# Performance work log

Measured on AMD Instinct MI355X. Metric: run time of the kernel, lower is better.

Reference implementation:

```python
import jax, jax.numpy as jnp
import numpy as np

B = 512; S = 6; Q = 2            # meta-batch, n_way*k_shot, n_way*q_query
DIM = 64; IMG = 28; N_WAY = 2
HEADS = 4; HD = DIM // HEADS     # retrieval heads / head dim
EPS = 1e-5


def _pool_mat(inp, out):
    # exact torch AdaptiveAvgPool2d windowing as a matrix [out, inp]
    P = np.zeros((out, inp), np.float32)
    for i in range(out):
        s = (i * inp) // out
        e = -((-(i + 1) * inp) // out)
        P[i, s:e] = 1.0 / (e - s)
    return jnp.asarray(P)

P28 = _pool_mat(IMG, 8)  # 28 -> 8; subsequent 8 -> 8 pools are identity


def _gelu(x):
    return jax.nn.gelu(x, approximate=False)


def _conv(x, w, b):
    y = jax.lax.conv_general_dilated(x, w, (1, 1), ((1, 1), (1, 1)),
                                     dimension_numbers=('NCHW', 'OIHW', 'NCHW'))
    return y + b[None, :, None, None]


def _bn(x, p):
    # p rows: gamma, beta, running_mean, running_var (eval-mode BatchNorm2d)
    g, bt, m, v = p[0], p[1], p[2], p[3]
    sc = g / jnp.sqrt(v + EPS)
    return (x - m[None, :, None, None]) * sc[None, :, None, None] + bt[None, :, None, None]


def _img_in(x, c1w, c1b, bn1, c2w, c2b, bn2, c3w, c3b, bn3, c4w, c4b, bn4, lin_w):
    h = _bn(_conv(x, c1w, c1b), bn1)
    h = jnp.einsum('oi,ncij,pj->ncop', P28, h, P28)   # adaptive avg pool 28x28 -> 8x8
    h = _gelu(h)                                       # dropout is identity in eval
    h = _gelu(_bn(_conv(h, c2w, c2b), bn2))
    h = _gelu(_bn(_conv(h, c3w, c3b), bn3))
    h = _gelu(_bn(_conv(h, c4w, c4b), bn4))            # -> [N,1,8,8]
    h = h.reshape(h.shape[0], -1)                      # [N,64]
    return h @ lin_w.T                                 # Linear(64 -> DIM, no bias)


def _net(x, w1, w2):
    # x: [B,K,D]; w1,w2: [B,D,D] batched fast weights
    h = jnp.einsum('bed,bkd->bke', w1, x)
    ah = _gelu(h)
    y = jnp.einsum('bed,bkd->bke', w2, ah)
    return y, h


def _get_lor(x, w1, w2, r_q, r_k, r_v, r_o, ln_w, ln_b):
    b, k, _ = x.shape
    q, _ = _net(x, w1, w2)
    qh = jnp.einsum('nhd,bkd->bknh', r_q, q)
    sc = jnp.einsum('bknh,rnh->bknr', qh, r_k) / (HD ** 0.5)
    p = jax.nn.softmax(sc, axis=-1)
    lor = jnp.einsum('bknr,rnh->bknh', p, r_v).reshape(b, k, DIM)
    lor = jnp.einsum('de,bkd->bke', r_o, lor)
    z = lor + x
    mu = z.mean(-1, keepdims=True)
    var = ((z - mu) ** 2).mean(-1, keepdims=True)
    return (z - mu) / jnp.sqrt(var + EPS) * ln_w + ln_b


def _forward(query_w, sxs, qxs, inner_lr, c1w, c1b, bn1, c2w, c2b, bn2, c3w, c3b, bn3,
             c4w, c4b, bn4, lin_w, emb, w1, w2, tags, r_q, r_k, r_v, r_o, ln_w, ln_b,
             sys, qys):
    b = query_w.shape[0]
    s = sxs.shape[1]
    q = qxs.shape[1]
    feats = lambda im: _img_in(im.reshape(-1, 1, IMG, IMG), c1w, c1b, bn1, c2w, c2b,
                               bn2, c3w, c3b, bn3, c4w, c4b, bn4, lin_w)
    sx = feats(sxs).reshape(b, s, DIM)
    qx = feats(qxs).reshape(b, q, DIM)
    qe = tags[4]
    w1b = jnp.broadcast_to(w1, (b, DIM, DIM))
    w2b = jnp.broadcast_to(w2, (b, DIM, DIM))
    bound = sx + emb[sys]                                          # [B,S,D]
    # all 4 tag variants for all S shots in one vectorized get_lor call
    inp = (bound[:, :, None, :] + tags[:4][None, None]).reshape(b, s * 4, DIM)
    lors = _get_lor(inp, w1b, w2b, r_q, r_k, r_v, r_o, ln_w, ln_b).reshape(b, s, 4, DIM)
    l1s, r1s, l2s, r2s = lors[:, :, 0], lors[:, :, 1], lors[:, :, 2], lors[:, :, 3]
    qw1 = w1[None] + jnp.einsum('bsl,bsr->blr', l1s, r1s)
    qw2 = w2[None] + jnp.einsum('bsl,bsr->blr', l2s, r2s)
    preds, _ = _net(qx + qe, qw1, qw2)                             # [B,Q,D]
    logits = jnp.einsum('ld,bqd->bql', emb, preds).reshape(-1, N_WAY)
    labels = qys.reshape(-1)
    ls = jax.nn.log_softmax(logits)
    task_loss = -jnp.take_along_axis(ls, labels[:, None], axis=1).mean()
    n_correct = (jnp.argmax(logits, axis=1) == labels).sum()
    return task_loss, n_correct, b * q


def setup_inputs() -> dict:
    key = jax.random.key(0)
    ks = jax.random.split(key, 24)
    rn = lambda i, sh, sc=1.0: sc * jax.random.normal(ks[i], sh, jnp.float32)
    def bnp(i, c):
        k0, k1, k2 = jax.random.split(ks[i], 3)
        return jnp.stack([1.0 + 0.1 * jax.random.normal(k0, (c,)),
                          0.1 * jax.random.normal(k1, (c,)),
                          0.1 * jax.random.normal(k2, (c,)),
                          0.5 + jax.random.uniform(jax.random.fold_in(ks[i], 3), (c,))])
    return {
        'query_w': rn(0, (B, DIM)),
        'sxs': rn(1, (B, S, IMG * IMG)),
        'qxs': rn(2, (B, Q, IMG * IMG)),
        'inner_lr': jnp.float32(0.1),
        'c1w': rn(3, (32, 1, 3, 3), 0.3), 'c1b': rn(4, (32,), 0.1), 'bn1': bnp(5, 32),
        'c2w': rn(6, (32, 32, 3, 3), 0.06), 'c2b': rn(7, (32,), 0.1), 'bn2': bnp(8, 32),
        'c3w': rn(9, (32, 32, 3, 3), 0.06), 'c3b': rn(10, (32,), 0.1), 'bn3': bnp(11, 32),
        'c4w': rn(12, (1, 32, 3, 3), 0.06), 'c4b': rn(13, (1,), 0.1), 'bn4': bnp(14, 1),
        'lin_w': rn(15, (DIM, 64), 0.125),
        'emb': rn(16, (N_WAY, DIM), 0.125),
        'w1': rn(17, (DIM, DIM), 0.125),
        'w2': rn(18, (DIM, DIM), 0.125),
        'tags': rn(19, (8, DIM), 0.125),
        'r_q': rn(20, (HEADS, HD, DIM), 0.125),
        'r_k': rn(21, (16, HEADS, HD), 0.25),
        'r_v': rn(22, (16, HEADS, HD), 0.25),
        'r_o': rn(23, (DIM, DIM), 0.125),
        'ln_w': 0.001 * jnp.ones((DIM,), jnp.float32),
        'ln_b': jnp.zeros((DIM,), jnp.float32),
        'sys': jax.random.randint(jax.random.fold_in(key, 100), (B, S), 0, N_WAY),
        'qys': jax.random.randint(jax.random.fold_in(key, 101), (B, Q), 0, N_WAY),
    }


def reference(query_w, sxs, qxs, inner_lr, c1w, c1b, bn1, c2w, c2b, bn2, c3w, c3b, bn3,
              c4w, c4b, bn4, lin_w, emb, w1, w2, tags, r_q, r_k, r_v, r_o, ln_w, ln_b,
              sys, qys):
    task_loss, n_correct, n_q = _forward(query_w, sxs, qxs, inner_lr, c1w, c1b, bn1,
                                         c2w, c2b, bn2, c3w, c3b, bn3, c4w, c4b, bn4,
                                         lin_w, emb, w1, w2, tags, r_q, r_k, r_v, r_o,
                                         ln_w, ln_b, sys, qys)
    return (task_loss, task_loss, jnp.float32(0.0), n_correct, n_q)
```

## Files before the change

kernel.cpp:

```cpp
#include <hip/hip_runtime.h>
#include <math.h>

constexpr int NSUP = 3072;
constexpr float EPSF = 1e-5f;

constexpr int WS_W1B  = 0;
constexpr int WS_B1   = 1024;
constexpr int WS_W2B  = 1056;
constexpr int WS_W3B  = 5664;
constexpr int WS_W4B  = 10272;
constexpr int WS_B4   = 10416;
constexpr int WS_B2   = 10420;
constexpr int WS_B3   = 10452;
constexpr int WS_HW1  = 10484;
constexpr int WS_HW2  = 12788;
constexpr int WS_HRQ  = 15092;
constexpr int WS_HROT = 17396;
constexpr int WS_RKB  = 19700;
constexpr int WS_RVT  = 20212;
constexpr int WS_PART = 20724;
constexpr int WS_FEATS= 21748;

using short8 = __attribute__((ext_vector_type(8))) short;
using f32x4  = __attribute__((ext_vector_type(4))) float;

__device__ __forceinline__ float gelu_f(float x) {
    float z  = fabsf(x) * 0.70710678118654752440f;
    float t  = __builtin_amdgcn_rcpf(__builtin_fmaf(0.3275911f, z, 1.0f));
    float p  = t * __builtin_fmaf(t,
                 __builtin_fmaf(t,
                   __builtin_fmaf(t,
                     __builtin_fmaf(t, 1.061405429f, -1.453152027f),
                     1.421413741f),
                   -0.284496736f),
                 0.254829592f);
    float e  = __expf(-z * z);
// ... 8 lines not shown
__device__ __forceinline__ float bflo(unsigned u) { return __uint_as_float(u << 16); }
__device__ __forceinline__ float bfhi(unsigned u) { return __uint_as_float(u & 0xffff0000u); }

__global__ void __launch_bounds__(256) precompute_kernel(
    const float* __restrict__ c1w, const float* __restrict__ c1b, const float* __restrict__ bn1,
    const float* __restrict__ c2w, const float* __restrict__ c2b, const float* __restrict__ bn2,
    const float* __restrict__ c3w, const float* __restrict__ c3b, const float* __restrict__ bn3,
    const float* __restrict__ c4w, const float* __restrict__ c4b, const float* __restrict__ bn4,
    const float* __restrict__ w1, const float* __restrict__ w2,
    const float* __restrict__ rq, const float* __restrict__ ro,
    const float* __restrict__ rk, const float* __restrict__ rv,
    float* __restrict__ ws)
{
    const int gid = blockIdx.x * 256 + threadIdx.x;
    const int gsz = gridDim.x * 256;

    unsigned short* w1b = (unsigned short*)(ws + WS_W1B);
    for (int v = gid; v < 2048; v += gsz) {
        int c8 = v & 7, colx = (v >> 3) & 15, qd = (v >> 7) & 3, hh = (v >> 9) & 1, kt = v >> 10;
        int tap = kt * 32 + qd * 8 + c8;
        int oc = hh * 16 + colx;
        unsigned short o = 0;
        if (tap < 36) {
            int tt = tap / 6, s = tap - tt * 6;
            float sum = 0.f;
            for (int di = 0; di < 3; ++di) {
                int a = tt - di; if (a < 0 || a > 3) continue;
                for (int dj = 0; dj < 3; ++dj) {
                    int bb = s - dj; if (bb < 0 || bb > 3) continue;
                    sum += c1w[oc * 9 + di * 3 + dj];
// ... 21 lines not shown
        float sc2 = bn2[oc] * rsqrtf(bn2[96 + oc] + EPSF);
        float sc3 = bn3[oc] * rsqrtf(bn3[96 + oc] + EPSF);
        w2b[v] = f2bf(c2w[oc * 288 + ic * 9 + tap] * sc2);
        w3b[v] = f2bf(c3w[oc * 288 + ic * 9 + tap] * sc3);
    }
    {
        unsigned short* w4b = (unsigned short*)(ws + WS_W4B);
        float sc4 = bn4[0] * rsqrtf(bn4[3] + EPSF);
        for (int v = gid; v < 288; v += gsz) {
            int tap = v >> 5, ic = v & 31;
            w4b[v] = f2bf(c4w[ic * 9 + tap] * sc4);
        }
        if (gid == 0) ws[WS_B4] = (c4b[0] - bn4[2]) * sc4 + bn4[1];
    }
    unsigned short* hw1 = (unsigned short*)(ws + WS_HW1);
    unsigned short* hw2 = (unsigned short*)(ws + WS_HW2);
    unsigned short* hrq = (unsigned short*)(ws + WS_HRQ);
    unsigned short* hro = (unsigned short*)(ws + WS_HROT);
    for (int v = gid; v < 4608; v += gsz) {
        int e = v / 72, d = v - e * 72;
        unsigned short a = 0, b = 0, c = 0, r = 0;
        if (d < 64) {
            a = f2bf(w1[e * 64 + d]);
            b = f2bf(w2[e * 64 + d]);
            c = f2bf(rq[e * 64 + d]);
            r = f2bf(ro[d * 64 + e]);
        }
        hw1[v] = a; hw2[v] = b; hrq[v] = c; hro[v] = r;
    }
    unsigned short* rkb = (unsigned short*)(ws + WS_RKB);
    unsigned short* rvt = (unsigned short*)(ws + WS_RVT);
    for (int v = gid; v < 1024; v += gsz) {
        int nn = v >> 8, x = (v >> 4) & 15, y = v & 15;
        rkb[v] = f2bf(rk[x * 64 + nn * 16 + y] * 0.25f);
        rvt[v] = f2bf(rv[y * 64 + nn * 16 + x]);
    }
}

__device__ __forceinline__ void conv32g(const unsigned short* __restrict__ A,
                                        const unsigned short* __restrict__ Wg,
                                        int col, int quad, f32x4 (&acc)[4][2])
{
    int ab[4];
    #pragma unroll
    for (int mt = 0; mt < 4; ++mt) {
        int px = mt * 16 + col;
        ab[mt] = quad * 800 + ((px >> 3) * 10 + (px & 7)) * 8;
        acc[mt][0] = (f32x4){0,0,0,0};
        acc[mt][1] = (f32x4){0,0,0,0};
    }
    #pragma unroll
    for (int dr = 0; dr < 3; ++dr)
// ... 14 lines not shown
__device__ __forceinline__ void conv_store4(unsigned short* __restrict__ A,
                                            const f32x4 (&acc)[4][2],
                                            float bi0, float bi1, int col, int quad)
{
    #pragma unroll
    for (int mt = 0; mt < 4; ++mt)
        #pragma unroll
        for (int reg = 0; reg < 4; ++reg) {
            int px = mt * 16 + quad * 4 + reg;
            int P = ((px >> 3) + 1) * 10 + (px & 7) + 1;
            A[(col >> 3) * 800 + P * 8 + (col & 7)]       = f2bf(gelu_f(acc[mt][0][reg] + bi0));
            A[(2 + (col >> 3)) * 800 + P * 8 + (col & 7)] = f2bf(gelu_f(acc[mt][1][reg] + bi1));
        }
}

__global__ void __launch_bounds__(256, 4) feats_kernel(
    const float* __restrict__ sxs, const float* __restrict__ qxs,
    const float* __restrict__ lin_w, const float* __restrict__ ws,
    float* __restrict__ feats)
{
    __shared__ __align__(16) unsigned short sAct[4][3200];
    __shared__ __align__(16) float sh4[4][64];

    const int t    = threadIdx.x;
    const int wv   = t >> 6;
    const int lane = t & 63;
    const int col  = lane & 15;
    const int quad = lane >> 4;
    const int n    = blockIdx.x * 4 + wv;

    unsigned short* A = sAct[wv];

    float bi1a = ws[WS_B1 + col], bi1b = ws[WS_B1 + 16 + col];
    float bi2a = ws[WS_B2 + col], bi2b = ws[WS_B2 + 16 + col];
    float bi3a = ws[WS_B3 + col], bi3b = ws[WS_B3 + 16 + col];
    float b4   = ws[WS_B4];

    {
        const float* img = (n < NSUP) ? (sxs + (size_t)n * 784) : (qxs + (size_t)(n - NSUP) * 784);
        const float4* sv = (const float4*)img;
        #pragma unroll
        for (int j = 0; j < 4; ++j) {
            int idx = j * 64 + lane;
            if (idx < 196) {
                float4 v = sv[idx];
                ushort4 o = { f2bf(v.x), f2bf(v.y), f2bf(v.z), f2bf(v.w) };
                *(ushort4*)(A + idx * 4) = o;
            }
        }
    }

    f32x4 acc[4][2];
    {
        const unsigned short* w1g = (const unsigned short*)(ws + WS_W1B);
        short8 b00 = *(const short8*)(w1g + ((0 * 4 + quad) * 16 + col) * 8);
        short8 b01 = *(const short8*)(w1g + ((1 * 4 + quad) * 16 + col) * 8);
        short8 b10 = *(const short8*)(w1g + ((2 * 4 + quad) * 16 + col) * 8);
        short8 b11 = *(const short8*)(w1g + ((3 * 4 + quad) * 16 + col) * 8);
        int ttj[8], ssj[8];
        #pragma unroll
        for (int j = 0; j < 8; ++j) {
            int k = quad * 8 + j;
            ttj[j] = k / 6; ssj[j] = k - ttj[j] * 6;
        }
        #pragma unroll
        for (int mt = 0; mt < 4; ++mt) {
            acc[mt][0] = (f32x4){0,0,0,0};
            acc[mt][1] = (f32x4){0,0,0,0};
            int px = mt * 16 + col;
            int sr = (((px >> 3) * 7) >> 1) - 1;
            int sc = (((px & 7) * 7) >> 1) - 1;
            short8 a0;
            #pragma unroll
            for (int j = 0; j < 8; ++j) {
                int rr = sr + ttj[j], cc = sc + ssj[j];
                bool ok = ((unsigned)rr < 28u) && ((unsigned)cc < 28u);
                int off = ok ? (rr * 28 + cc) : 0;
                unsigned short hv = A[off];
                a0[j] = ok ? (short)hv : (short)0;
            }
            acc[mt][0] = __builtin_amdgcn_mfma_f32_16x16x32_bf16(a0, b00, acc[mt][0], 0, 0, 0);
            acc[mt][1] = __builtin_amdgcn_mfma_f32_16x16x32_bf16(a0, b01, acc[mt][1], 0, 0, 0);
            short8 a1 = {0,0,0,0,0,0,0,0};
            if (quad == 0) {
                #pragma unroll
                for (int j = 0; j < 4; ++j) {
                    int rr = sr + 5, cc = sc + 2 + j;
                    bool ok = ((unsigned)rr < 28u) && ((unsigned)cc < 28u);
                    int off = ok ? (rr * 28 + cc) : 0;
                    unsigned short hv = A[off];
                    a1[j] = ok ? (short)hv : (short)0;
                }
            }
            acc[mt][0] = __builtin_amdgcn_mfma_f32_16x16x32_bf16(a1, b10, acc[mt][0], 0, 0, 0);
            acc[mt][1] = __builtin_amdgcn_mfma_f32_16x16x32_bf16(a1, b11, acc[mt][1], 0, 0, 0);
        }
    }
    {
        uint4 z4 = {0, 0, 0, 0};
        #pragma unroll
        for (int it = 0; it < 3; ++it) {
            int h = lane + it * 64;
            if (h < 144) {
                int pi = h >> 2, ch = h & 3;
                int P;
                if (pi < 10)      P = pi;
                else if (pi < 20) P = 90 + (pi - 10);
                else { int k = pi - 20; int r = 1 + (k >> 1); P = r * 10 + (k & 1) * 9; }
                ((uint4*)A)[ch * 100 + P] = z4;
            }
        }
    }
    conv_store4(A, acc, bi1a, bi1b, col, quad);

    conv32g(A, (const unsigned short*)(ws + WS_W2B), col, quad, acc);
    conv_store4(A, acc, bi2a, bi2b, col, quad);
    conv32g(A, (const unsigned short*)(ws + WS_W3B), col, quad, acc);
    conv_store4(A, acc, bi3a, bi3b, col, quad);

    {
        f32x4 acc4[4];
        int ab[4];
        #pragma unroll
        for (int mt = 0; mt < 4; ++mt) {
            int px = mt * 16 + col;
            ab[mt] = quad * 800 + ((px >> 3) * 10 + (px & 7)) * 8;
            acc4[mt] = (f32x4){0,0,0,0};
        }
        const unsigned short* w4g = (const unsigned short*)(ws + WS_W4B);
        #pragma unroll
        for (int dr = 0; dr < 3; ++dr)
            #pragma unroll
            for (int dc = 0; dc < 3; ++dc) {
                int tap = dr * 3 + dc;
                short8 b = *(const short8*)(w4g + tap * 32 + quad * 8);
                #pragma unroll
                for (int mt = 0; mt < 4; ++mt) {
                    short8 a = *(const short8*)(A + ab[mt] + (dr * 10 + dc) * 8);
                    acc4[mt] = __builtin_amdgcn_mfma_f32_16x16x32_bf16(a, b, acc4[mt], 0, 0, 0);
                }
            }
        if (col < 4) {
            f32x4 v = acc4[0];
            if (col == 1) v = acc4[1];
            else if (col == 2) v = acc4[2];
            else if (col == 3) v = acc4[3];
            #pragma unroll
            for (int reg = 0; reg < 4; ++reg)
                sh4[wv][col * 16 + quad * 4 + reg] = gelu_f(v[reg] + b4);
        }
    }

    {
        const float4* lw = (const float4*)(lin_w + (size_t)lane * 64);
        const float4* hp = (const float4*)sh4[wv];
        float acc2 = 0.f;
        #pragma unroll
        for (int j = 0; j < 16; ++j) {
            float4 w = lw[j], h = hp[j];
            acc2 += w.x * h.x + w.y * h.y + w.z * h.z + w.w * h.w;
        }
        feats[n * 64 + lane] = acc2;
    }
}

__device__ __forceinline__ void head_gemm(const unsigned short* __restrict__ Ab,
                                          const unsigned short* __restrict__ Bw,
                                          int col, int quad, int wvid, f32x4 res[2])
{
    #pragma unroll
    for (int u = 0; u < 2; ++u) {
        int tau = wvid + u * 4;
        int mt = tau & 1, nt = tau >> 1;
        f32x4 acc = {0, 0, 0, 0};
        #pragma unroll
        for (int kt = 0; kt < 2; ++kt) {
            short8 a = *(const short8*)(Ab + (mt * 16 + col) * 72 + kt * 32 + quad * 8);
            short8 b = *(const short8*)(Bw + (nt * 16 + col) * 72 + kt * 32 + quad * 8);
            acc = __builtin_amdgcn_mfma_f32_16x16x32_bf16(a, b, acc, 0, 0, 0);
        }
        res[u] = acc;
    }
}

__global__ void __launch_bounds__(256, 2) head_kernel(
    const float* __restrict__ emb, const float* __restrict__ tags,
    const float* __restrict__ lnw, const float* __restrict__ lnb,
    const int* __restrict__ sys, const int* __restrict__ qys,
    const float* __restrict__ ws, const float* __restrict__ feats,
    float* __restrict__ part)
{
    __shared__ __align__(16) unsigned short sW1B[4608], sW2B[4608], sRQB[4608], sROT[4608];
    __shared__ __align__(16) unsigned short bufA[2304], bufB[2304];
    __shared__ __align__(16) unsigned short sP[2048];
    __shared__ __align__(16) float sXf[1536];
    __shared__ __align__(16) float s_xq[128], s_ah[128], s_yp[128];
    __shared__ float s_t1[12], s_t2[12], s_mu[24], s_rs[24], s_lg[4];

    const int t    = threadIdx.x;
    const int b    = blockIdx.x;
    const int wvid = t >> 6;
    const int col  = t & 15;
    const int quad = (t >> 4) & 3;

    for (int i = t; i < 576; i += 256) {
        ((uint4*)sW1B)[i] = ((const uint4*)(ws + WS_HW1))[i];
        ((uint4*)sW2B)[i] = ((const uint4*)(ws + WS_HW2))[i];
        ((uint4*)sRQB)[i] = ((const uint4*)(ws + WS_HRQ))[i];
        ((uint4*)sROT)[i] = ((const uint4*)(ws + WS_HROT))[i];
    }
    {
        uint4 z = {0, 0, 0, 0};
        if (t < 72) {
            ((uint4*)(bufA + 1728))[t] = z;
            ((uint4*)(bufB + 1728))[t] = z;
        }
        if (t < 64)
            ((uint4*)(sP + 1536))[t] = z;
    }
    for (int idx = t; idx < 1536; idx += 256) {
        int k = idx >> 6, e = idx & 63;
        int s = k >> 2, tg = k & 3;
        int cls = sys[b * 6 + s];
        float v = feats[(b * 6 + s) * 64 + e] + emb[cls * 64 + e] + tags[tg * 64 + e];
        sXf[idx] = v;
        bufA[k * 72 + e] = f2bf(v);
    }
    __syncthreads();

    f32x4 r[2];
    head_gemm(bufA, sW1B, col, quad, wvid, r);
    #pragma unroll
    for (int u = 0; u < 2; ++u) {
        int tau = wvid + u * 4, mt = tau & 1, nt = tau >> 1;
        #pragma unroll
        for (int reg = 0; reg < 4; ++reg) {
            int row = mt * 16 + quad * 4 + reg;
            if (row < 24) bufB[row * 72 + nt * 16 + col] = f2bf(gelu_f(r[u][reg]));
        }
    }
    __syncthreads();
    head_gemm(bufB, sW2B, col, quad, wvid, r);
    #pragma unroll
    for (int u = 0; u < 2; ++u) {
        int tau = wvid + u * 4, mt = tau & 1, nt = tau >> 1;
        #pragma unroll
        for (int reg = 0; reg < 4; ++reg) {
            int row = mt * 16 + quad * 4 + reg;
            if (row < 24) bufA[row * 72 + nt * 16 + col] = f2bf(r[u][reg]);
        }
    }
    __syncthreads();
    head_gemm(bufA, sRQB, col, quad, wvid, r);
    #pragma unroll
    for (int u = 0; u < 2; ++u) {
        int tau = wvid + u * 4, mt = tau & 1, nt = tau >> 1;
        #pragma unroll
        for (int reg = 0; reg < 4; ++reg) {
            int row = mt * 16 + quad * 4 + reg;
            if (row < 24) bufB[row * 72 + nt * 16 + col] = f2bf(r[u][reg]);
        }
    }
    __syncthreads();

    {
        const int nh = wvid;
        const unsigned short* rkB = (const unsigned short*)(ws + WS_RKB) + nh * 256;
        const unsigned short* rvT = (const unsigned short*)(ws + WS_RVT) + nh * 256;
        const short8 zz = {0,0,0,0,0,0,0,0};
        const bool lo = (quad < 2);
        short8 bK = lo ? *(const short8*)(rkB + col * 16 + quad * 8) : zz;
        short8 a0 = lo ? *(const short8*)(bufB + col * 72 + nh * 16 + quad * 8) : zz;
        short8 a1 = lo ? *(const short8*)(bufB + (16 + col) * 72 + nh * 16 + quad * 8) : zz;
        f32x4 s0 = __builtin_amdgcn_mfma_f32_16x16x32_bf16(a0, bK, (f32x4){0,0,0,0}, 0, 0, 0);
        f32x4 s1 = __builtin_amdgcn_mfma_f32_16x16x32_bf16(a1, bK, (f32x4){0,0,0,0}, 0, 0, 0);
        #pragma unroll
        for (int reg = 0; reg < 4; ++reg) {
            float v = s0[reg];
            float m = v;
            m = fmaxf(m, __shfl_xor(m, 1)); m = fmaxf(m, __shfl_xor(m, 2));
            m = fmaxf(m, __shfl_xor(m, 4)); m = fmaxf(m, __shfl_xor(m, 8));
            float p = __expf(v - m);
            float su = p;
            su += __shfl_xor(su, 1); su += __shfl_xor(su, 2);
            su += __shfl_xor(su, 4); su += __shfl_xor(su, 8);
            sP[(quad * 4 + reg) * 64 + nh * 16 + col] = f2bf(p / su);
            v = s1[reg];
            m = v;
// ... 7 lines not shown
        }
        short8 bV  = lo ? *(const short8*)(rvT + col * 16 + quad * 8) : zz;
        short8 pa0 = lo ? *(const short8*)(sP + col * 64 + nh * 16 + quad * 8) : zz;
        short8 pa1 = lo ? *(const short8*)(sP + (16 + col) * 64 + nh * 16 + quad * 8) : zz;
        f32x4 o0 = __builtin_amdgcn_mfma_f32_16x16x32_bf16(pa0, bV, (f32x4){0,0,0,0}, 0, 0, 0);
        f32x4 o1 = __builtin_amdgcn_mfma_f32_16x16x32_bf16(pa1, bV, (f32x4){0,0,0,0}, 0, 0, 0);
        #pragma unroll
        for (int reg = 0; reg < 4; ++reg) {
            bufA[(quad * 4 + reg) * 72 + nh * 16 + col] = f2bf(o0[reg]);
            int tok = 16 + quad * 4 + reg;
            if (tok < 24) bufA[tok * 72 + nh * 16 + col] = f2bf(o1[reg]);
        }
    }
    __syncthreads();

    head_gemm(bufA, sROT, col, quad, wvid, r);
    #pragma unroll
    for (int u = 0; u < 2; ++u) {
        int tau = wvid + u * 4, mt = tau & 1, nt = tau >> 1;
        #pragma unroll
        for (int reg = 0; reg < 4; ++reg) {
            int row = mt * 16 + quad * 4 + reg;
            if (row < 24) {
                int idx = row * 64 + nt * 16 + col;
                sXf[idx] = sXf[idx] + r[u][reg];
            }
        }
    }
    __syncthreads();

    if (t < 192) {
        int k = t >> 3, j = t & 7;
        const float4* zp = (const float4*)(sXf + k * 64 + j * 8);
        float4 v0 = zp[0], v1 = zp[1];
        float sx_ = v0.x + v0.y + v0.z + v0.w + v1.x + v1.y + v1.z + v1.w;
        sx_ += __shfl_xor(sx_, 1); sx_ += __shfl_xor(sx_, 2); sx_ += __shfl_xor(sx_, 4);
        float mu = sx_ * (1.0f / 64.0f);
        float d0 = v0.x - mu, d1 = v0.y - mu, d2 = v0.z - mu, d3 = v0.w - mu;
        float d4 = v1.x - mu, d5 = v1.y - mu, d6 = v1.z - mu, d7 = v1.w - mu;
        float vv = d0*d0 + d1*d1 + d2*d2 + d3*d3 + d4*d4 + d5*d5 + d6*d6 + d7*d7;
        vv += __shfl_xor(vv, 1); vv += __shfl_xor(vv, 2); vv += __shfl_xor(vv, 4);
        if (j == 0) {
            s_mu[k] = mu;
            s_rs[k] = 1.0f / sqrtf(vv * (1.0f / 64.0f) + EPSF);
        }
    }
    __syncthreads();
    for (int idx = t; idx < 1536; idx += 256) {
        int k = idx >> 6, e = idx & 63;
        float v = (sXf[idx] - s_mu[k]) * s_rs[k] * lnw[e] + lnb[e];
        bufB[k * 72 + e] = f2bf(v);
    }
    if (t < 128) {
        int q = t >> 6, e = t & 63;
        s_xq[t] = feats[(NSUP + b * 2 + q) * 64 + e] + tags[256 + e];
    }
    __syncthreads();

    if (t < 96) {
        int idx = t >> 3, j = t & 7;
        int q = idx / 6, s = idx - q * 6;
        uint4 u = ((const uint4*)(bufB + (s * 4 + 1) * 72))[j];
        const float* x = s_xq + q * 64 + j * 8;
        float d = bflo(u.x)*x[0] + bfhi(u.x)*x[1] + bflo(u.y)*x[2] + bfhi(u.y)*x[3]
                + bflo(u.z)*x[4] + bfhi(u.z)*x[5] + bflo(u.w)*x[6] + bfhi(u.w)*x[7];
        d += __shfl_xor(d, 1); d += __shfl_xor(d, 2); d += __shfl_xor(d, 4);
        if (j == 0) s_t1[idx] = d;
    }
    __syncthreads();
    if (t < 128) {
        int q = t >> 6, e = t & 63;
        const uint4* wp = (const uint4*)(sW1B + e * 72);
        const float* xp = s_xq + q * 64;
        float acc = 0.f;
        #pragma unroll
        for (int j = 0; j < 8; ++j) {
            uint4 u = wp[j];
            const float* x = xp + j * 8;
            acc += bflo(u.x)*x[0] + bfhi(u.x)*x[1] + bflo(u.y)*x[2] + bfhi(u.y)*x[3]
                 + bflo(u.z)*x[4] + bfhi(u.z)*x[5] + bflo(u.w)*x[6] + bfhi(u.w)*x[7];
        }
        #pragma unroll
        for (int s = 0; s < 6; ++s)
            acc += bflo((unsigned)bufB[(s * 4 + 0) * 72 + e]) * s_t1[q * 6 + s];
        s_ah[t] = gelu_f(acc);
    }
    __syncthreads();
    if (t < 96) {
        int idx = t >> 3, j = t & 7;
        int q = idx / 6, s = idx - q * 6;
        uint4 u = ((const uint4*)(bufB + (s * 4 + 3) * 72))[j];
        const float* x = s_ah + q * 64 + j * 8;
        float d = bflo(u.x)*x[0] + bfhi(u.x)*x[1] + bflo(u.y)*x[2] + bfhi(u.y)*x[3]
                + bflo(u.z)*x[4] + bfhi(u.z)*x[5] + bflo(u.w)*x[6] + bfhi(u.w)*x[7];
        d += __shfl_xor(d, 1); d += __shfl_xor(d, 2); d += __shfl_xor(d, 4);
        if (j == 0) s_t2[idx] = d;
    }
    __syncthreads();
    if (t < 128) {
        int q = t >> 6, e = t & 63;
        const uint4* wp = (const uint4*)(sW2B + e * 72);
        const float* xp = s_ah + q * 64;
        float acc = 0.f;
        #pragma unroll
        for (int j = 0; j < 8; ++j) {
            uint4 u = wp[j];
            const float* x = xp + j * 8;
            acc += bflo(u.x)*x[0] + bfhi(u.x)*x[1] + bflo(u.y)*x[2] + bfhi(u.y)*x[3]
                 + bflo(u.z)*x[4] + bfhi(u.z)*x[5] + bflo(u.w)*x[6] + bfhi(u.w)*x[7];
        }
        #pragma unroll
        for (int s = 0; s < 6; ++s)
            acc += bflo((unsigned)bufB[(s * 4 + 2) * 72 + e]) * s_t2[q * 6 + s];
        s_yp[t] = acc;
    }
    __syncthreads();
    if (t < 32) {
        int q = t >> 4, ll = (t >> 3) & 1, j = t & 7;
        const float* ep = emb + ll * 64 + j * 8;
        const float* yp = s_yp + q * 64 + j * 8;
        float d = ep[0]*yp[0] + ep[1]*yp[1] + ep[2]*yp[2] + ep[3]*yp[3]
                + ep[4]*yp[4] + ep[5]*yp[5] + ep[6]*yp[6] + ep[7]*yp[7];
        d += __shfl_xor(d, 1); d += __shfl_xor(d, 2); d += __shfl_xor(d, 4);
        if (j == 0) s_lg[q * 2 + ll] = d;
    }
    __syncthreads();
    if (t == 0) {
        float lsum = 0.f, corr = 0.f;
        #pragma unroll
        for (int q = 0; q < 2; ++q) {
            float l0 = s_lg[q * 2], l1 = s_lg[q * 2 + 1];
            int lab = qys[b * 2 + q];
            float m = fmaxf(l0, l1);
            float lse = m + logf(expf(l0 - m) + expf(l1 - m));
            lsum += -((lab ? l1 : l0) - lse);
            int pred = (l1 > l0) ? 1 : 0;
            corr += (pred == lab) ? 1.0f : 0.0f;
        }
        part[b] = lsum;
        part[512 + b] = corr;
    }
}

__global__ void __launch_bounds__(256) finalize_kernel(const float* __restrict__ part,
                                                       float* __restrict__ out)
{
    __shared__ float sl[256], sc[256];
    const int t = threadIdx.x;
    sl[t] = part[t] + part[t + 256];
    sc[t] = part[512 + t] + part[768 + t];
    __syncthreads();
    for (int s = 128; s > 0; s >>= 1) {
        if (t < s) { sl[t] += sl[t + s]; sc[t] += sc[t + s]; }
        __syncthreads();
    }
    if (t == 0) {
        float loss = sl[0] * (1.0f / 1024.0f);
        out[0] = loss;
        out[1] = loss;
        out[2] = 0.0f;
        out[3] = sc[0];
        out[4] = 1024.0f;
    }
}

extern "C" void kernel_launch(void* const* d_in, const int* in_sizes, int n_in,
                              void* d_out, int out_size, void* d_ws, size_t ws_size,
                              hipStream_t stream)
{
    (void)in_sizes; (void)n_in; (void)out_size; (void)ws_size;
    const float* sxs  = (const float*)d_in[1];
    const float* qxs  = (const float*)d_in[2];
    const float* c1w  = (const float*)d_in[4];
    const float* c1b  = (const float*)d_in[5];
    const float* bn1  = (const float*)d_in[6];
    const float* c2w  = (const float*)d_in[7];
    const float* c2b  = (const float*)d_in[8];
// ... 12 lines not shown
    const float* rq   = (const float*)d_in[21];
    const float* rk   = (const float*)d_in[22];
    const float* rv   = (const float*)d_in[23];
    const float* ro   = (const float*)d_in[24];
    const float* lnw  = (const float*)d_in[25];
    const float* lnb  = (const float*)d_in[26];
    const int*   sys  = (const int*)d_in[27];
    const int*   qys  = (const int*)d_in[28];

    float* ws  = (float*)d_ws;
    float* out = (float*)d_out;

    precompute_kernel<<<64, 256, 0, stream>>>(c1w, c1b, bn1, c2w, c2b, bn2,
                                              c3w, c3b, bn3, c4w, c4b, bn4,
                                              w1, w2, rq, ro, rk, rv, ws);
    feats_kernel<<<1024, 256, 0, stream>>>(sxs, qxs, lin_w, ws, ws + WS_FEATS);
    head_kernel<<<512, 256, 0, stream>>>(emb, tags, lnw, lnb, sys, qys,
                                         ws, ws + WS_FEATS, ws + WS_PART);
    finalize_kernel<<<1, 256, 0, stream>>>(ws + WS_PART, out);
}
```

Before: 167.8 us.

## Fuse feature extraction, head, and finalize into one per-task kernel

Merges the conv feature kernel, the per-task head kernel and the final reduction into a single 512-thread kernel per meta-batch task. Each of the eight waves extracts one image's features straight into shared memory, so the global feats round trip and two launches go away. The last block, found through an atomic counter, does the final reduction. The rq·w2 product is also folded into a precomputed matrix, which removes one head GEMM stage. In exchange, shared memory per block grows via a union, and the finalize step now relies on threadfence and atomic ordering.

```diff
diff --git a/kernel.cpp b/kernel.cpp
--- a/kernel.cpp
+++ b/kernel.cpp
@@ -1,7 +1,6 @@
 #include <hip/hip_runtime.h>
 #include <math.h>
 
-constexpr int NSUP = 3072;
 constexpr float EPSF = 1e-5f;
 
 constexpr int WS_W1B  = 0;
@@ -13,13 +12,13 @@
 constexpr int WS_B2   = 10420;
 constexpr int WS_B3   = 10452;
 constexpr int WS_HW1  = 10484;
-constexpr int WS_HW2  = 12788;
-constexpr int WS_HRQ  = 15092;
+constexpr int WS_HM   = 12788;
+constexpr int WS_HW2  = 15092;
 constexpr int WS_HROT = 17396;
 constexpr int WS_RKB  = 19700;
 constexpr int WS_RVT  = 20212;
 constexpr int WS_PART = 20724;
-constexpr int WS_FEATS= 21748;
+constexpr int WS_CNT  = 21748;
 
 using short8 = __attribute__((ext_vector_type(8))) short;
 using f32x4  = __attribute__((ext_vector_type(4))) float;
@@ -58,6 +57,8 @@
 {
     const int gid = blockIdx.x * 256 + threadIdx.x;
     const int gsz = gridDim.x * 256;
+
+    if (gid == 0) *((unsigned*)(ws + WS_CNT)) = 0u;
 
     unsigned short* w1b = (unsigned short*)(ws + WS_W1B);
     for (int v = gid; v < 2048; v += gsz) {
@@ -109,8 +110,8 @@
         if (gid == 0) ws[WS_B4] = (c4b[0] - bn4[2]) * sc4 + bn4[1];
     }
     unsigned short* hw1 = (unsigned short*)(ws + WS_HW1);
+    unsigned short* hm  = (unsigned short*)(ws + WS_HM);
     unsigned short* hw2 = (unsigned short*)(ws + WS_HW2);
-    unsigned short* hrq = (unsigned short*)(ws + WS_HRQ);
     unsigned short* hro = (unsigned short*)(ws + WS_HROT);
     for (int v = gid; v < 4608; v += gsz) {
         int e = v / 72, d = v - e * 72;
@@ -118,10 +119,12 @@
         if (d < 64) {
             a = f2bf(w1[e * 64 + d]);
             b = f2bf(w2[e * 64 + d]);
-            c = f2bf(rq[e * 64 + d]);
+            float m = 0.f;
+            for (int q = 0; q < 64; ++q) m += rq[e * 64 + q] * w2[q * 64 + d];
+            c = f2bf(m);
             r = f2bf(ro[d * 64 + e]);
         }
-        hw1[v] = a; hw2[v] = b; hrq[v] = c; hro[v] = r;
+        hw1[v] = a; hw2[v] = b; hm[v] = c; hro[v] = r;
     }
     unsigned short* rkb = (unsigned short*)(ws + WS_RKB);
     unsigned short* rvt = (unsigned short*)(ws + WS_RVT);
@@ -131,6 +134,24 @@
         rvt[v] = f2bf(rv[y * 64 + nn * 16 + x]);
     }
 }
+
+struct FeatsSmem {
+    unsigned short sAct[8][3200];
+    float          sh4[8][64];
+};
+struct HeadSmem {
+    unsigned short sW1B[4608];
+    unsigned short sM[4608];
+    unsigned short sW2B[4608];
+    unsigned short sROT[4608];
+    unsigned short bufA[2304];
+    unsigned short bufB[2304];
+    unsigned short sP[2048];
+};
+union FusedSmem {
+    FeatsSmem f;
+    HeadSmem  h;
+};
 
 __device__ __forceinline__ void conv32g(const unsigned short* __restrict__ A,
                                         const unsigned short* __restrict__ Wg,
@@ -175,264 +196,240 @@
         }
 }
 
-__global__ void __launch_bounds__(256, 4) feats_kernel(
+__device__ __forceinline__ f32x4 head_gemm8(const unsigned short* __restrict__ Ab,
+                                            const unsigned short* __restrict__ Bw,
+                                            int col, int quad, int wvid)
+{
+    int mt = wvid & 1, nt = wvid >> 1;
+    f32x4 acc = {0, 0, 0, 0};
+    #pragma unroll
+    for (int kt = 0; kt < 2; ++kt) {
+        short8 a = *(const short8*)(Ab + (mt * 16 + col) * 72 + kt * 32 + quad * 8);
+        short8 b = *(const short8*)(Bw + (nt * 16 + col) * 72 + kt * 32 + quad * 8);
+        acc = __builtin_amdgcn_mfma_f32_16x16x32_bf16(a, b, acc, 0, 0, 0);
+    }
+    return acc;
+}
+
+__global__ void __launch_bounds__(512, 4) fused_kernel(
     const float* __restrict__ sxs, const float* __restrict__ qxs,
-    const float* __restrict__ lin_w, const float* __restrict__ ws,
-    float* __restrict__ feats)
+    const float* __restrict__ lin_w,
+    const float* __restrict__ emb, const float* __restrict__ tags,
+    const float* __restrict__ lnw, const float* __restrict__ lnb,
+    const int* __restrict__ sys, const int* __restrict__ qys,
+    float* __restrict__ ws, float* __restrict__ out)
 {
-    __shared__ __align__(16) unsigned short sAct[4][3200];
-    __shared__ __align__(16) float sh4[4][64];
+    __shared__ __align__(16) FusedSmem sm;
+    __shared__ __align__(16) float sFeat[8][64];
+    __shared__ __align__(16) float sXf[1536];
+    __shared__ __align__(16) float s_xq[128], s_ah[128], s_yp[128];
+    __shared__ float s_t1[12], s_t2[12], s_mu[24], s_rs[24], s_lg[4], s_red[16];
+    __shared__ int s_last;
 
     const int t    = threadIdx.x;
+    const int b    = blockIdx.x;
     const int wv   = t >> 6;
     const int lane = t & 63;
     const int col  = lane & 15;
     const int quad = lane >> 4;
-    const int n    = blockIdx.x * 4 + wv;
-
-    unsigned short* A = sAct[wv];
-
-    float bi1a = ws[WS_B1 + col], bi1b = ws[WS_B1 + 16 + col];
-    float bi2a = ws[WS_B2 + col], bi2b = ws[WS_B2 + 16 + col];
-    float bi3a = ws[WS_B3 + col], bi3b = ws[WS_B3 + 16 + col];
-    float b4   = ws[WS_B4];
 
     {
-        const float* img = (n < NSUP) ? (sxs + (size_t)n * 784) : (qxs + (size_t)(n - NSUP) * 784);
-        const float4* sv = (const float4*)img;
-        #pragma unroll
-        for (int j = 0; j < 4; ++j) {
-            int idx = j * 64 + lane;
-            if (idx < 196) {
-                float4 v = sv[idx];
-                ushort4 o = { f2bf(v.x), f2bf(v.y), f2bf(v.z), f2bf(v.w) };
-                *(ushort4*)(A + idx * 4) = o;
-            }
-        }
-    }
-
-    f32x4 acc[4][2];
-    {
-        const unsigned short* w1g = (const unsigned short*)(ws + WS_W1B);
-        short8 b00 = *(const short8*)(w1g + ((0 * 4 + quad) * 16 + col) * 8);
-        short8 b01 = *(const short8*)(w1g + ((1 * 4 + quad) * 16 + col) * 8);
-        short8 b10 = *(const short8*)(w1g + ((2 * 4 + quad) * 16 + col) * 8);
-        short8 b11 = *(const short8*)(w1g + ((3 * 4 + quad) * 16 + col) * 8);
-        int ttj[8], ssj[8];
-        #pragma unroll
-        for (int j = 0; j < 8; ++j) {
-            int k = quad * 8 + j;
-            ttj[j] = k / 6; ssj[j] = k - ttj[j] * 6;
-        }
-        #pragma unroll
-        for (int mt = 0; mt < 4; ++mt) {
-            acc[mt][0] = (f32x4){0,0,0,0};
-            acc[mt][1] = (f32x4){0,0,0,0};
-            int px = mt * 16 + col;
-            int sr = (((px >> 3) * 7) >> 1) - 1;
-            int sc = (((px & 7) * 7) >> 1) - 1;
-            short8 a0;
+        unsigned short* A = sm.f.sAct[wv];
+        float bi1a = ws[WS_B1 + col], bi1b = ws[WS_B1 + 16 + col];
+        float bi2a = ws[WS_B2 + col], bi2b = ws[WS_B2 + 16 + col];
+        float bi3a = ws[WS_B3 + col], bi3b = ws[WS_B3 + 16 + col];
+        float b4   = ws[WS_B4];
+
+        {
+            const float* img = (wv < 6) ? (sxs + ((size_t)b * 6 + wv) * 784)
+                                        : (qxs + ((size_t)b * 2 + (wv - 6)) * 784);
+            const float4* sv = (const float4*)img;
+            #pragma unroll
+            for (int j = 0; j < 4; ++j) {
+                int idx = j * 64 + lane;
+                if (idx < 196) {
+                    float4 v = sv[idx];
+                    ushort4 o = { f2bf(v.x), f2bf(v.y), f2bf(v.z), f2bf(v.w) };
+                    *(ushort4*)(A + idx * 4) = o;
+                }
+            }
+        }
+
+        f32x4 acc[4][2];
+        {
+            const unsigned short* w1g = (const unsigned short*)(ws + WS_W1B);
+            short8 b00 = *(const short8*)(w1g + ((0 * 4 + quad) * 16 + col) * 8);
+            short8 b01 = *(const short8*)(w1g + ((1 * 4 + quad) * 16 + col) * 8);
+            short8 b10 = *(const short8*)(w1g + ((2 * 4 + quad) * 16 + col) * 8);
+            short8 b11 = *(const short8*)(w1g + ((3 * 4 + quad) * 16 + col) * 8);
+            int ttj[8], ssj[8];
             #pragma unroll
             for (int j = 0; j < 8; ++j) {
-                int rr = sr + ttj[j], cc = sc + ssj[j];
-                bool ok = ((unsigned)rr < 28u) && ((unsigned)cc < 28u);
-                int off = ok ? (rr * 28 + cc) : 0;
-                unsigned short hv = A[off];
-                a0[j] = ok ? (short)hv : (short)0;
-            }
-            acc[mt][0] = __builtin_amdgcn_mfma_f32_16x16x32_bf16(a0, b00, acc[mt][0], 0, 0, 0);
-            acc[mt][1] = __builtin_amdgcn_mfma_f32_16x16x32_bf16(a0, b01, acc[mt][1], 0, 0, 0);
-            short8 a1 = {0,0,0,0,0,0,0,0};
-            if (quad == 0) {
+                int k = quad * 8 + j;
+                ttj[j] = k / 6; ssj[j] = k - ttj[j] * 6;
+            }
+            #pragma unroll
+            for (int mt = 0; mt < 4; ++mt) {
+                acc[mt][0] = (f32x4){0,0,0,0};
+                acc[mt][1] = (f32x4){0,0,0,0};
+                int px = mt * 16 + col;
+                int sr = (((px >> 3) * 7) >> 1) - 1;
+                int sc = (((px & 7) * 7) >> 1) - 1;
+                short8 a0;
                 #pragma unroll
-                for (int j = 0; j < 4; ++j) {
-                    int rr = sr + 5, cc = sc + 2 + j;
+                for (int j = 0; j < 8; ++j) {
+                    int rr = sr + ttj[j], cc = sc + ssj[j];
                     bool ok = ((unsigned)rr < 28u) && ((unsigned)cc < 28u);
                     int off = ok ? (rr * 28 + cc) : 0;
                     unsigned short hv = A[off];
-                    a1[j] = ok ? (short)hv : (short)0;
+                    a0[j] = ok ? (short)hv : (short)0;
                 }
-            }
-            acc[mt][0] = __builtin_amdgcn_mfma_f32_16x16x32_bf16(a1, b10, acc[mt][0], 0, 0, 0);
-            acc[mt][1] = __builtin_amdgcn_mfma_f32_16x16x32_bf16(a1, b11, acc[mt][1], 0, 0, 0);
-        }
-    }
-    {
-        uint4 z4 = {0, 0, 0, 0};
-        #pragma unroll
-        for (int it = 0; it < 3; ++it) {
-            int h = lane + it * 64;
-            if (h < 144) {
-                int pi = h >> 2, ch = h & 3;
-                int P;
-                if (pi < 10)      P = pi;
-                else if (pi < 20) P = 90 + (pi - 10);
-                else { int k = pi - 20; int r = 1 + (k >> 1); P = r * 10 + (k & 1) * 9; }
-                ((uint4*)A)[ch * 100 + P] = z4;
-            }
-        }
-    }
-    conv_store4(A, acc, bi1a, bi1b, col, quad);
-
-    conv32g(A, (const unsigned short*)(ws + WS_W2B), col, quad, acc);
-    conv_store4(A, acc, bi2a, bi2b, col, quad);
-    conv32g(A, (const unsigned short*)(ws + WS_W3B), col, quad, acc);
-    conv_store4(A, acc, bi3a, bi3b, col, quad);
-
-    {
-        f32x4 acc4[4];
-        int ab[4];
-        #pragma unroll
-        for (int mt = 0; mt < 4; ++mt) {
-            int px = mt * 16 + col;
-            ab[mt] = quad * 800 + ((px >> 3) * 10 + (px & 7)) * 8;
-            acc4[mt] = (f32x4){0,0,0,0};
-        }
-        const unsigned short* w4g = (const unsigned short*)(ws + WS_W4B);
-        #pragma unroll
-        for (int dr = 0; dr < 3; ++dr)
-            #pragma unroll
-            for (int dc = 0; dc < 3; ++dc) {
-                int tap = dr * 3 + dc;
-                short8 b = *(const short8*)(w4g + tap * 32 + quad * 8);
+                acc[mt][0] = __builtin_amdgcn_mfma_f32_16x16x32_bf16(a0, b00, acc[mt][0], 0, 0, 0);
+                acc[mt][1] = __builtin_amdgcn_mfma_f32_16x16x32_bf16(a0, b01, acc[mt][1], 0, 0, 0);
+                short8 a1 = {0,0,0,0,0,0,0,0};
+                if (quad == 0) {
+                    #pragma unroll
+                    for (int j = 0; j < 4; ++j) {
+                        int rr = sr + 5, cc = sc + 2 + j;
+                        bool ok = ((unsigned)rr < 28u) && ((unsigned)cc < 28u);
+                        int off = ok ? (rr * 28 + cc) : 0;
+                        unsigned short hv = A[off];
+                        a1[j] = ok ? (short)hv : (short)0;
+                    }
+                }
+                acc[mt][0] = __builtin_amdgcn_mfma_f32_16x16x32_bf16(a1, b10, acc[mt][0], 0, 0, 0);
+                acc[mt][1] = __builtin_amdgcn_mfma_f32_16x16x32_bf16(a1, b11, acc[mt][1], 0, 0, 0);
+            }
+        }
+        {
+            uint4 z4 = {0, 0, 0, 0};
+            #pragma unroll
+            for (int it = 0; it < 3; ++it) {
+                int h = lane + it * 64;
+                if (h < 144) {
+                    int pi = h >> 2, ch = h & 3;
+                    int P;
+                    if (pi < 10)      P = pi;
+                    else if (pi < 20) P = 90 + (pi - 10);
+                    else { int k = pi - 20; int r = 1 + (k >> 1); P = r * 10 + (k & 1) * 9; }
+                    ((uint4*)A)[ch * 100 + P] = z4;
+                }
+            }
+        }
+        conv_store4(A, acc, bi1a, bi1b, col, quad);
+
+        conv32g(A, (const unsigned short*)(ws + WS_W2B), col, quad, acc);
+        conv_store4(A, acc, bi2a, bi2b, col, quad);
+        conv32g(A, (const unsigned short*)(ws + WS_W3B), col, quad, acc);
+        conv_store4(A, acc, bi3a, bi3b, col, quad);
+
+        {
+            f32x4 acc4[4];
+            int ab[4];
+            #pragma unroll
+            for (int mt = 0; mt < 4; ++mt) {
+                int px = mt * 16 + col;
+                ab[mt] = quad * 800 + ((px >> 3) * 10 + (px & 7)) * 8;
+                acc4[mt] = (f32x4){0,0,0,0};
+            }
+            const unsigned short* w4g = (const unsigned short*)(ws + WS_W4B);
+            #pragma unroll
+            for (int dr = 0; dr < 3; ++dr)
                 #pragma unroll
-                for (int mt = 0; mt < 4; ++mt) {
-                    short8 a = *(const short8*)(A + ab[mt] + (dr * 10 + dc) * 8);
-                    acc4[mt] = __builtin_amdgcn_mfma_f32_16x16x32_bf16(a, b, acc4[mt], 0, 0, 0);
+                for (int dc = 0; dc < 3; ++dc) {
+                    int tap = dr * 3 + dc;
+                    short8 bb = *(const short8*)(w4g + tap * 32 + quad * 8);
+                    #pragma unroll
+                    for (int mt = 0; mt < 4; ++mt) {
+                        short8 a = *(const short8*)(A + ab[mt] + (dr * 10 + dc) * 8);
+                        acc4[mt] = __builtin_amdgcn_mfma_f32_16x16x32_bf16(a, bb, acc4[mt], 0, 0, 0);
+                    }
                 }
-            }
-        if (col < 4) {
-            f32x4 v = acc4[0];
-            if (col == 1) v = acc4[1];
-            else if (col == 2) v = acc4[2];
-            else if (col == 3) v = acc4[3];
-            #pragma unroll
-            for (int reg = 0; reg < 4; ++reg)
-                sh4[wv][col * 16 + quad * 4 + reg] = gelu_f(v[reg] + b4);
-        }
-    }
-
-    {
-        const float4* lw = (const float4*)(lin_w + (size_t)lane * 64);
-        const float4* hp = (const float4*)sh4[wv];
-        float acc2 = 0.f;
-        #pragma unroll
-        for (int j = 0; j < 16; ++j) {
-            float4 w = lw[j], h = hp[j];
-            acc2 += w.x * h.x + w.y * h.y + w.z * h.z + w.w * h.w;
-        }
-        feats[n * 64 + lane] = acc2;
-    }
-}
-
-__device__ __forceinline__ void head_gemm(const unsigned short* __restrict__ Ab,
-                                          const unsigned short* __restrict__ Bw,
-                                          int col, int quad, int wvid, f32x4 res[2])
-{
-    #pragma unroll
-    for (int u = 0; u < 2; ++u) {
-        int tau = wvid + u * 4;
-        int mt = tau & 1, nt = tau >> 1;
-        f32x4 acc = {0, 0, 0, 0};
-        #pragma unroll
-        for (int kt = 0; kt < 2; ++kt) {
-            short8 a = *(const short8*)(Ab + (mt * 16 + col) * 72 + kt * 32 + quad * 8);
-            short8 b = *(const short8*)(Bw + (nt * 16 + col) * 72 + kt * 32 + quad * 8);
-            acc = __builtin_amdgcn_mfma_f32_16x16x32_bf16(a, b, acc, 0, 0, 0);
-        }
-        res[u] = acc;
-    }
-}
-
-__global__ void __launch_bounds__(256, 2) head_kernel(
-    const float* __restrict__ emb, const float* __restrict__ tags,
-    const float* __restrict__ lnw, const float* __restrict__ lnb,
-    const int* __restrict__ sys, const int* __restrict__ qys,
-    const float* __restrict__ ws, const float* __restrict__ feats,
-    float* __restrict__ part)
-{
-    __shared__ __align__(16) unsigned short sW1B[4608], sW2B[4608], sRQB[4608], sROT[4608];
-    __shared__ __align__(16) unsigned short bufA[2304], bufB[2304];
-    __shared__ __align__(16) unsigned short sP[2048];
-    __shared__ __align__(16) float sXf[1536];
-    __shared__ __align__(16) float s_xq[128], s_ah[128], s_yp[128];
-    __shared__ float s_t1[12], s_t2[12], s_mu[24], s_rs[24], s_lg[4];
-
-    const int t    = threadIdx.x;
-    const int b    = blockIdx.x;
-    const int wvid = t >> 6;
-    const int col  = t & 15;
-    const int quad = (t >> 4) & 3;
-
-    for (int i = t; i < 576; i += 256) {
-        ((uint4*)sW1B)[i] = ((const uint4*)(ws + WS_HW1))[i];
-        ((uint4*)sW2B)[i] = ((const uint4*)(ws + WS_HW2))[i];
-        ((uint4*)sRQB)[i] = ((const uint4*)(ws + WS_HRQ))[i];
-        ((uint4*)sROT)[i] = ((const uint4*)(ws + WS_HROT))[i];
-    }
-    {
+            if (col < 4) {
+                f32x4 v = acc4[0];
+                if (col == 1) v = acc4[1];
+                else if (col == 2) v = acc4[2];
+                else if (col == 3) v = acc4[3];
+                #pragma unroll
+                for (int reg = 0; reg < 4; ++reg)
+                    sm.f.sh4[wv][col * 16 + quad * 4 + reg] = gelu_f(v[reg] + b4);
+            }
+        }
+        {
+            const float4* lw = (const float4*)(lin_w + (size_t)lane * 64);
+            const float4* hp = (const float4*)sm.f.sh4[wv];
+            float acc2 = 0.f;
+            #pragma unroll
+            for (int j = 0; j < 16; ++j) {
+                float4 w = lw[j], h = hp[j];
+                acc2 += w.x * h.x + w.y * h.y + w.z * h.z + w.w * h.w;
+            }
+            sFeat[wv][lane] = acc2;
+        }
+    }
+    __syncthreads();
+
+    for (int i = t; i < 576; i += 512) {
+        ((uint4*)sm.h.sW1B)[i] = ((const uint4*)(ws + WS_HW1))[i];
+        ((uint4*)sm.h.sM)[i]   = ((const uint4*)(ws + WS_HM))[i];
+        ((uint4*)sm.h.sW2B)[i] = ((const uint4*)(ws + WS_HW2))[i];
+        ((uint4*)sm.h.sROT)[i] = ((const uint4*)(ws + WS_HROT))[i];
+    }
+    if (t < 72) {
         uint4 z = {0, 0, 0, 0};
-        if (t < 72) {
-            ((uint4*)(bufA + 1728))[t] = z;
-            ((uint4*)(bufB + 1728))[t] = z;
-        }
-        if (t < 64)
-            ((uint4*)(sP + 1536))[t] = z;
-    }
-    for (int idx = t; idx < 1536; idx += 256) {
+        ((uint4*)(sm.h.bufA + 1728))[t] = z;
+        ((uint4*)(sm.h.bufB + 1728))[t] = z;
+    }
+    for (int idx = t; idx < 1536; idx += 512) {
         int k = idx >> 6, e = idx & 63;
         int s = k >> 2, tg = k & 3;
         int cls = sys[b * 6 + s];
-        float v = feats[(b * 6 + s) * 64 + e] + emb[cls * 64 + e] + tags[tg * 64 + e];
+        float v = sFeat[s][e] + emb[cls * 64 + e] + tags[tg * 64 + e];
         sXf[idx] = v;
-        bufA[k * 72 + e] = f2bf(v);
-    }
-    __syncthreads();
-
-    f32x4 r[2];
-    head_gemm(bufA, sW1B, col, quad, wvid, r);
-    #pragma unroll
-    for (int u = 0; u < 2; ++u) {
-        int tau = wvid + u * 4, mt = tau & 1, nt = tau >> 1;
+        sm.h.bufA[k * 72 + e] = f2bf(v);
+    }
+    if (t < 128) {
+        int q = t >> 6, e = t & 63;
+        s_xq[t] = sFeat[6 + q][e] + tags[256 + e];
+    }
+    __syncthreads();
+
+    {
+        f32x4 r = head_gemm8(sm.h.bufA, sm.h.sW1B, col, quad, wv);
+        int mt = wv & 1, nt = wv >> 1;
         #pragma unroll
         for (int reg = 0; reg < 4; ++reg) {
             int row = mt * 16 + quad * 4 + reg;
-            if (row < 24) bufB[row * 72 + nt * 16 + col] = f2bf(gelu_f(r[u][reg]));
-        }
-    }
-    __syncthreads();
-    head_gemm(bufB, sW2B, col, quad, wvid, r);
-    #pragma unroll
-    for (int u = 0; u < 2; ++u) {
-        int tau = wvid + u * 4, mt = tau & 1, nt = tau >> 1;
+            if (row < 24) sm.h.bufB[row * 72 + nt * 16 + col] = f2bf(gelu_f(r[reg]));
+        }
+    }
+    __syncthreads();
+    {
+        f32x4 r = head_gemm8(sm.h.bufB, sm.h.sM, col, quad, wv);
+        int mt = wv & 1, nt = wv >> 1;
         #pragma unroll
         for (int reg = 0; reg < 4; ++reg) {
             int row = mt * 16 + quad * 4 + reg;
-            if (row < 24) bufA[row * 72 + nt * 16 + col] = f2bf(r[u][reg]);
-        }
-    }
-    __syncthreads();
-    head_gemm(bufA, sRQB, col, quad, wvid, r);
-    #pragma unroll
-    for (int u = 0; u < 2; ++u) {
-        int tau = wvid + u * 4, mt = tau & 1, nt = tau >> 1;
-        #pragma unroll
-        for (int reg = 0; reg < 4; ++reg) {
-            int row = mt * 16 + quad * 4 + reg;
-            if (row < 24) bufB[row * 72 + nt * 16 + col] = f2bf(r[u][reg]);
-        }
-    }
-    __syncthreads();
-
-    {
-        const int nh = wvid;
+            if (row < 24) sm.h.bufA[row * 72 + nt * 16 + col] = f2bf(r[reg]);
+        }
+    }
+    __syncthreads();
+
+    if (wv < 4) {
+        const int nh = wv;
         const unsigned short* rkB = (const unsigned short*)(ws + WS_RKB) + nh * 256;
         const unsigned short* rvT = (const unsigned short*)(ws + WS_RVT) + nh * 256;
+        unsigned short* bufA = sm.h.bufA;
+        unsigned short* sP   = sm.h.sP;
         const short8 zz = {0,0,0,0,0,0,0,0};
         const bool lo = (quad < 2);
+        {
+            int r8 = lane >> 3, c2 = lane & 7;
+            *(unsigned int*)(sP + (24 + r8) * 64 + nh * 16 + c2 * 2) = 0u;
+        }
         short8 bK = lo ? *(const short8*)(rkB + col * 16 + quad * 8) : zz;
-        short8 a0 = lo ? *(const short8*)(bufB + col * 72 + nh * 16 + quad * 8) : zz;
-        short8 a1 = lo ? *(const short8*)(bufB + (16 + col) * 72 + nh * 16 + quad * 8) : zz;
+        short8 a0 = lo ? *(const short8*)(bufA + col * 72 + nh * 16 + quad * 8) : zz;
+        short8 a1 = lo ? *(const short8*)(bufA + (16 + col) * 72 + nh * 16 + quad * 8) : zz;
         f32x4 s0 = __builtin_amdgcn_mfma_f32_16x16x32_bf16(a0, bK, (f32x4){0,0,0,0}, 0, 0, 0);
         f32x4 s1 = __builtin_amdgcn_mfma_f32_16x16x32_bf16(a1, bK, (f32x4){0,0,0,0}, 0, 0, 0);
         #pragma unroll
@@ -470,16 +467,15 @@
     }
     __syncthreads();
 
-    head_gemm(bufA, sROT, col, quad, wvid, r);
-    #pragma unroll
-    for (int u = 0; u < 2; ++u) {
-        int tau = wvid + u * 4, mt = tau & 1, nt = tau >> 1;
+    {
+        f32x4 r = head_gemm8(sm.h.bufA, sm.h.sROT, col, quad, wv);
+        int mt = wv & 1, nt = wv >> 1;
         #pragma unroll
         for (int reg = 0; reg < 4; ++reg) {
             int row = mt * 16 + quad * 4 + reg;
             if (row < 24) {
                 int idx = row * 64 + nt * 16 + col;
-                sXf[idx] = sXf[idx] + r[u][reg];
+                sXf[idx] = sXf[idx] + r[reg];
             }
         }
     }
@@ -502,21 +498,17 @@
         }
     }
     __syncthreads();
-    for (int idx = t; idx < 1536; idx += 256) {
+    for (int idx = t; idx < 1536; idx += 512) {
         int k = idx >> 6, e = idx & 63;
         float v = (sXf[idx] - s_mu[k]) * s_rs[k] * lnw[e] + lnb[e];
-        bufB[k * 72 + e] = f2bf(v);
-    }
-    if (t < 128) {
-        int q = t >> 6, e = t & 63;
-        s_xq[t] = feats[(NSUP + b * 2 + q) * 64 + e] + tags[256 + e];
+        sm.h.bufB[k * 72 + e] = f2bf(v);
     }
     __syncthreads();
 
     if (t < 96) {
         int idx = t >> 3, j = t & 7;
         int q = idx / 6, s = idx - q * 6;
-        uint4 u = ((const uint4*)(bufB + (s * 4 + 1) * 72))[j];
+        uint4 u = ((const uint4*)(sm.h.bufB + (s * 4 + 1) * 72))[j];
         const float* x = s_xq + q * 64 + j * 8;
         float d = bflo(u.x)*x[0] + bfhi(u.x)*x[1] + bflo(u.y)*x[2] + bfhi(u.y)*x[3]
                 + bflo(u.z)*x[4] + bfhi(u.z)*x[5] + bflo(u.w)*x[6] + bfhi(u.w)*x[7];
@@ -526,7 +518,7 @@
     __syncthreads();
     if (t < 128) {
         int q = t >> 6, e = t & 63;
-        const uint4* wp = (const uint4*)(sW1B + e * 72);
+        const uint4* wp = (const uint4*)(sm.h.sW1B + e * 72);
         const float* xp = s_xq + q * 64;
         float acc = 0.f;
         #pragma unroll
@@ -538,14 +530,14 @@
         }
         #pragma unroll
         for (int s = 0; s < 6; ++s)
-            acc += bflo((unsigned)bufB[(s * 4 + 0) * 72 + e]) * s_t1[q * 6 + s];
+            acc += bflo((unsigned)sm.h.bufB[(s * 4 + 0) * 72 + e]) * s_t1[q * 6 + s];
         s_ah[t] = gelu_f(acc);
     }
     __syncthreads();
     if (t < 96) {
         int idx = t >> 3, j = t & 7;
         int q = idx / 6, s = idx - q * 6;
-        uint4 u = ((const uint4*)(bufB + (s * 4 + 3) * 72))[j];
+        uint4 u = ((const uint4*)(sm.h.bufB + (s * 4 + 3) * 72))[j];
         const float* x = s_ah + q * 64 + j * 8;
         float d = bflo(u.x)*x[0] + bfhi(u.x)*x[1] + bflo(u.y)*x[2] + bfhi(u.y)*x[3]
                 + bflo(u.z)*x[4] + bfhi(u.z)*x[5] + bflo(u.w)*x[6] + bfhi(u.w)*x[7];
@@ -555,7 +547,7 @@
     __syncthreads();
     if (t < 128) {
         int q = t >> 6, e = t & 63;
-        const uint4* wp = (const uint4*)(sW2B + e * 72);
+        const uint4* wp = (const uint4*)(sm.h.sW2B + e * 72);
         const float* xp = s_ah + q * 64;
         float acc = 0.f;
         #pragma unroll
@@ -567,10 +559,12 @@
         }
         #pragma unroll
         for (int s = 0; s < 6; ++s)
-            acc += bflo((unsigned)bufB[(s * 4 + 2) * 72 + e]) * s_t2[q * 6 + s];
+            acc += bflo((unsigned)sm.h.bufB[(s * 4 + 2) * 72 + e]) * s_t2[q * 6 + s];
         s_yp[t] = acc;
     }
     __syncthreads();
+
+    float* part = ws + WS_PART;
     if (t < 32) {
         int q = t >> 4, ll = (t >> 3) & 1, j = t & 7;
         const float* ep = emb + ll * 64 + j * 8;
@@ -580,7 +574,6 @@
         d += __shfl_xor(d, 1); d += __shfl_xor(d, 2); d += __shfl_xor(d, 4);
         if (j == 0) s_lg[q * 2 + ll] = d;
     }
-    __syncthreads();
     if (t == 0) {
         float lsum = 0.f, corr = 0.f;
         #pragma unroll
@@ -595,28 +588,34 @@
         }
         part[b] = lsum;
         part[512 + b] = corr;
-    }
-}
-
-__global__ void __launch_bounds__(256) finalize_kernel(const float* __restrict__ part,
-                                                       float* __restrict__ out)
-{
-    __shared__ float sl[256], sc[256];
-    const int t = threadIdx.x;
-    sl[t] = part[t] + part[t + 256];
-    sc[t] = part[512 + t] + part[768 + t];
-    __syncthreads();
-    for (int s = 128; s > 0; s >>= 1) {
-        if (t < s) { sl[t] += sl[t + s]; sc[t] += sc[t + s]; }
+        __threadfence();
+        unsigned old = atomicAdd((unsigned*)(ws + WS_CNT), 1u);
+        s_last = (old == 511) ? 1 : 0;
+    }
+    __syncthreads();
+
+    if (s_last) {
+        __threadfence();
+        float l = part[t];
+        float c = part[512 + t];
+        #pragma unroll
+        for (int off = 1; off < 64; off <<= 1) {
+            l += __shfl_xor(l, off);
+            c += __shfl_xor(c, off);
+        }
+        if (lane == 0) { s_red[wv * 2] = l; s_red[wv * 2 + 1] = c; }
         __syncthreads();
-    }
-    if (t == 0) {
-        float loss = sl[0] * (1.0f / 1024.0f);
-        out[0] = loss;
-        out[1] = loss;
-        out[2] = 0.0f;
-        out[3] = sc[0];
-        out[4] = 1024.0f;
+        if (t == 0) {
+            float L = 0.f, C = 0.f;
+            #pragma unroll
+            for (int w = 0; w < 8; ++w) { L += s_red[w * 2]; C += s_red[w * 2 + 1]; }
+            float loss = L * (1.0f / 1024.0f);
+            out[0] = loss;
+            out[1] = loss;
+            out[2] = 0.0f;
+            out[3] = C;
+            out[4] = 1024.0f;
+        }
     }
 }
 
@@ -659,8 +658,6 @@
     precompute_kernel<<<64, 256, 0, stream>>>(c1w, c1b, bn1, c2w, c2b, bn2,
                                               c3w, c3b, bn3, c4w, c4b, bn4,
                                               w1, w2, rq, ro, rk, rv, ws);
-    feats_kernel<<<1024, 256, 0, stream>>>(sxs, qxs, lin_w, ws, ws + WS_FEATS);
-    head_kernel<<<512, 256, 0, stream>>>(emb, tags, lnw, lnb, sys, qys,
-                                         ws, ws + WS_FEATS, ws + WS_PART);
-    finalize_kernel<<<1, 256, 0, stream>>>(ws + WS_PART, out);
-}
+    fused_kernel<<<512, 512, 0, stream>>>(sxs, qxs, lin_w, emb, tags, lnw, lnb,
+                                          sys, qys, ws, out);
+}
```

Measured after the change: 174.0 us. 3.7% more time.
